# Kernel optimization log

Measured on AMD Instinct MI355X. Metric: run time of the kernel, lower is better.

The kernel has to match this reference:

```python
import jax, jax.numpy as jnp
import numpy as np

N = 300_000   # octree nodes at this depth
K = 27        # 3x3x3 deconv kernel taps
CIN = 32
COUT = 32
G = 8         # group norm groups
B = 8         # octrees in batch
EPS = 1e-5


def setup_inputs() -> dict:
    key = jax.random.key(0)
    k1, k2, k3, k4 = jax.random.split(key, 4)
    data = jax.random.normal(k1, (N, CIN), jnp.float32)
    neigh = jax.random.randint(k2, (N, K), 0, N, jnp.int32)          # neighbor index table
    batch_id = jnp.sort(jax.random.randint(k3, (N,), 0, B, jnp.int32))  # sorted per-node octree id
    weights = jax.random.normal(k4, (K, CIN, COUT), jnp.float32) * 0.05
    gamma = jnp.ones((COUT,), jnp.float32)
    beta = jnp.zeros((COUT,), jnp.float32)
    return dict(data=data, weights=weights, gamma=gamma, beta=beta,
                neigh=neigh, batch_id=batch_id, n_batch=B)


def _octree_group_norm(h, batch_id, gamma, beta, n_batch):
    # Per-octree (segment) group norm, following ocnn.OctreeGroupNorm:
    # count = n_nodes_per_octree * C/G; inv_count = 1/(count+eps);
    # per-group mean/var via scatter_add then within-group channel sum.
    Nn, C = h.shape
    Cg = C // G
    cnt = jax.ops.segment_sum(jnp.ones((Nn,), h.dtype), batch_id,
                              num_segments=n_batch) * (C / G)   # [B]
    inv_cnt = 1.0 / (cnt + EPS)
    s = jax.ops.segment_sum(h, batch_id, num_segments=n_batch)   # [B, C]
    mean_g = s.reshape(n_batch, G, Cg).sum(-1) * inv_cnt[:, None]  # [B, G]
    mean = jnp.repeat(mean_g, Cg, axis=1)                          # [B, C]
    hc = h - mean[batch_id]
    v = jax.ops.segment_sum(hc * hc, batch_id, num_segments=n_batch)
    var_g = v.reshape(n_batch, G, Cg).sum(-1) * inv_cnt[:, None]
    inv_std = jnp.repeat(1.0 / jnp.sqrt(var_g + EPS), Cg, axis=1)  # [B, C]
    return hc * inv_std[batch_id] * gamma + beta


def reference(data, weights, gamma, beta, neigh, batch_id, n_batch):
    # Octree deconv (stride=1): gather 27 neighbors, small matmul per tap, sum.
    x = data[neigh]                                # [N, K, Cin] irregular gather
    out = jnp.einsum('nki,kio->no', x, weights)    # [N, Cout]
    out = _octree_group_norm(out, batch_id, gamma, beta, n_batch)
    return jax.nn.relu(out)
```

## Files before the change

### kernel.cpp

```cpp
#include <hip/hip_runtime.h>
#include <math.h>

#define EPS 1e-5f

typedef __attribute__((ext_vector_type(8)))  short  short8;
typedef __attribute__((ext_vector_type(16))) float  floatx16;

__device__ __forceinline__ unsigned short f2bf(float f) {
    unsigned int u = __float_as_uint(f);
    unsigned int r = (u + 0x7FFFu + ((u >> 16) & 1u)) >> 16;
    return (unsigned short)r;
}
__device__ __forceinline__ float bf2f(unsigned short h) {
    return __uint_as_float(((unsigned int)h) << 16);
}

__global__ __launch_bounds__(256) void pack_data_kernel(
    const float* __restrict__ data, unsigned short* __restrict__ dpk, int N)
{
    const int e4 = blockIdx.x * 256 + threadIdx.x;
    if (e4 >= N * 8) return;
    const float4 v = ((const float4*)data)[e4];
    const int node = e4 >> 3;
    const int cq   = (e4 & 7) * 4;
    ushort4 hi, lo;
    hi.x = f2bf(v.x); lo.x = f2bf(v.x - bf2f(hi.x));
    hi.y = f2bf(v.y); lo.y = f2bf(v.y - bf2f(hi.y));
    hi.z = f2bf(v.z); lo.z = f2bf(v.z - bf2f(hi.z));
    hi.w = f2bf(v.w); lo.w = f2bf(v.w - bf2f(hi.w));
    unsigned short* row = dpk + (size_t)node * 64;
    *(ushort4*)(row + cq)      = hi;
    *(ushort4*)(row + 32 + cq) = lo;
}

__global__ __launch_bounds__(256) void pack_w_kernel(
    const float* __restrict__ W, unsigned short* __restrict__ whi,
    unsigned short* __restrict__ wlo)
{
    const int t = blockIdx.x * 256 + threadIdx.x;
    if (t >= 27 * 2 * 64) return;
    const int l  = t & 63;
    const int h  = (t >> 6) & 1;
    const int k  = t >> 7;
    const int n  = l & 31;
    const int cb = h * 16 + (l >> 5) * 8;
    ushort4 h0, h1, l0, l1;
    const float* wp = W + k * 1024 + n;
    float w0 = wp[(cb + 0) * 32], w1 = wp[(cb + 1) * 32];
    float w2 = wp[(cb + 2) * 32], w3 = wp[(cb + 3) * 32];
    float w4 = wp[(cb + 4) * 32], w5 = wp[(cb + 5) * 32];
    float w6 = wp[(cb + 6) * 32], w7 = wp[(cb + 7) * 32];
    h0.x = f2bf(w0); l0.x = f2bf(w0 - bf2f(h0.x));
    h0.y = f2bf(w1); l0.y = f2bf(w1 - bf2f(h0.y));
    h0.z = f2bf(w2); l0.z = f2bf(w2 - bf2f(h0.z));
    h0.w = f2bf(w3); l0.w = f2bf(w3 - bf2f(h0.w));
    h1.x = f2bf(w4); l1.x = f2bf(w4 - bf2f(h1.x));
    h1.y = f2bf(w5); l1.y = f2bf(w5 - bf2f(h1.y));
    h1.z = f2bf(w6); l1.z = f2bf(w6 - bf2f(h1.z));
    h1.w = f2bf(w7); l1.w = f2bf(w7 - bf2f(h1.w));
    *(ushort4*)(whi + (size_t)t * 8)     = h0;
    *(ushort4*)(whi + (size_t)t * 8 + 4) = h1;
    *(ushort4*)(wlo + (size_t)t * 8)     = l0;
    *(ushort4*)(wlo + (size_t)t * 8 + 4) = l1;
}

__global__ __launch_bounds__(256) void deconv_stats_kernel(
    const unsigned short* __restrict__ dpk, const unsigned short* __restrict__ whi,
    const unsigned short* __restrict__ wlo, const int* __restrict__ neigh,
    const int* __restrict__ batch_id, float* __restrict__ out,
    float* __restrict__ gs1, float* __restrict__ gs2, float* __restrict__ gcnt,
    int N)
{
    __shared__ float ls1[256];
    __shared__ float ls2[256];
    __shared__ float lcnt[8];

    const int t    = threadIdx.x;
    const int wv   = t >> 6;
    const int l    = t & 63;
    const int mrow = l & 31;
    const int half = l >> 5;
    const int wbase = blockIdx.x * 128 + wv * 32;
    const int node  = wbase + mrow;
    const int nc    = node < N ? node : N - 1;
    const long srow = (long)nc * 27;

    ls1[t] = 0.f;
    ls2[t] = 0.f;
    if (t < 8) lcnt[t] = 0.f;
    __syncthreads();

    floatx16 acc;
#pragma unroll
    for (int r = 0; r < 16; ++r) acc[r] = 0.f;

    int nidx = neigh[srow];

#pragma unroll 1
    for (int k = 0; k < 27; ++k) {
        const unsigned short* arow = dpk + (size_t)nidx * 64;
        const short8 a_h0 = *(const short8*)(arow + half * 8);
        const short8 a_h1 = *(const short8*)(arow + 16 + half * 8);
        const short8 a_l0 = *(const short8*)(arow + 32 + half * 8);
        const short8 a_l1 = *(const short8*)(arow + 48 + half * 8);
        const unsigned short* bb = whi + ((size_t)k * 128 + l) * 8;
        const unsigned short* bl = wlo + ((size_t)k * 128 + l) * 8;
        const short8 b_h0 = *(const short8*)(bb);
        const short8 b_h1 = *(const short8*)(bb + 512);
        const short8 b_l0 = *(const short8*)(bl);
        const short8 b_l1 = *(const short8*)(bl + 512);
        if (k < 26) nidx = neigh[srow + k + 1];

        acc = __builtin_amdgcn_mfma_f32_32x32x16_bf16(a_h0, b_h0, acc, 0, 0, 0);
        acc = __builtin_amdgcn_mfma_f32_32x32x16_bf16(a_h1, b_h1, acc, 0, 0, 0);
        acc = __builtin_amdgcn_mfma_f32_32x32x16_bf16(a_l0, b_h0, acc, 0, 0, 0);
        acc = __builtin_amdgcn_mfma_f32_32x32x16_bf16(a_l1, b_h1, acc, 0, 0, 0);
        acc = __builtin_amdgcn_mfma_f32_32x32x16_bf16(a_h0, b_l0, acc, 0, 0, 0);
        acc = __builtin_amdgcn_mfma_f32_32x32x16_bf16(a_h1, b_l1, acc, 0, 0, 0);
    }

    const int co = mrow;
#pragma unroll
    for (int r = 0; r < 16; ++r) {
        const int row = (r & 3) + 8 * (r >> 2) + 4 * half;
        const int n = wbase + row;
        if (n < N) out[(size_t)n * 32 + co] = acc[r];
    }

    bool fast = (wbase + 31 < N);
    int bfst = 0;
    if (fast) {
        bfst = batch_id[wbase];
        fast = (bfst == batch_id[wbase + 31]);
    }
    if (fast) {
        float s1 = 0.f, s2 = 0.f;
#pragma unroll
        for (int r = 0; r < 16; ++r) {
            const float v = acc[r];
            s1 += v;
            s2 += v * v;
        }
        atomicAdd(&ls1[bfst * 32 + co], s1);
        atomicAdd(&ls2[bfst * 32 + co], s2);
    } else {
#pragma unroll
        for (int r = 0; r < 16; ++r) {
            const int row = (r & 3) + 8 * (r >> 2) + 4 * half;
            const int n = wbase + row;
            if (n < N) {
                const int b = batch_id[n];
                const float v = acc[r];
                atomicAdd(&ls1[b * 32 + co], v);
                atomicAdd(&ls2[b * 32 + co], v * v);
            }
        }
    }
    if (half == 0) {
        const int n = wbase + mrow;
        if (n < N) atomicAdd(&lcnt[batch_id[n]], 1.0f);
    }
    __syncthreads();

    {
        float v;
        v = ls1[t]; if (v != 0.f) atomicAdd(&gs1[t], v);
        v = ls2[t]; if (v != 0.f) atomicAdd(&gs2[t], v);
        if (t < 8) { v = lcnt[t]; if (v != 0.f) atomicAdd(&gcnt[t], v); }
    }
}

__global__ __launch_bounds__(256) void gn_relu_kernel(
    float* __restrict__ out, const int* __restrict__ batch_id,
    const float* __restrict__ gs1, const float* __restrict__ gs2,
    const float* __restrict__ gcnt, const float* __restrict__ gamma,
    const float* __restrict__ beta, int N)
{
    const int idx = blockIdx.x * 256 + threadIdx.x;
    if (idx >= N * 8) return;
    const int n = idx >> 3;
    const int g = idx & 7;
    const int b = batch_id[n];

    const float cnt  = gcnt[b] * 4.0f;
    const float icnt = 1.0f / (cnt + EPS);
    const float4 s1 = *(const float4*)(gs1 + b * 32 + g * 4);
    const float4 s2 = *(const float4*)(gs2 + b * 32 + g * 4);
    const float S1 = s1.x + s1.y + s1.z + s1.w;
    const float S2 = s2.x + s2.y + s2.z + s2.w;
    const float m   = S1 * icnt;
    const float var = (S2 - 2.0f * m * S1 + cnt * m * m) * icnt;
    const float istd = rsqrtf(var + EPS);

    const float4 gm4 = *(const float4*)(gamma + g * 4);
    const float4 bt4 = *(const float4*)(beta + g * 4);
    float4 h = *(float4*)(out + (size_t)idx * 4);
    h.x = fmaxf((h.x - m) * istd * gm4.x + bt4.x, 0.f);
    h.y = fmaxf((h.y - m) * istd * gm4.y + bt4.y, 0.f);
    h.z = fmaxf((h.z - m) * istd * gm4.z + bt4.z, 0.f);
    h.w = fmaxf((h.w - m) * istd * gm4.w + bt4.w, 0.f);
    *(float4*)(out + (size_t)idx * 4) = h;
}

extern "C" void kernel_launch(void* const* d_in, const int* in_sizes, int n_in,
                              void* d_out, int out_size, void* d_ws, size_t ws_size,
                              hipStream_t stream) {
    const float* data     = (const float*)d_in[0];
    const float* weights  = (const float*)d_in[1];
    const float* gamma    = (const float*)d_in[2];
    const float* beta     = (const float*)d_in[3];
    const int*   neigh    = (const int*)d_in[4];
    const int*   batch_id = (const int*)d_in[5];
    const int N = in_sizes[0] / 32;
    float* out = (float*)d_out;

    char* wsb = (char*)d_ws;
    float* gs1  = (float*)wsb;
    float* gs2  = gs1 + 256;
    float* gcnt = gs1 + 512;
    unsigned short* dpk = (unsigned short*)(wsb + 4096);
    unsigned short* whi = (unsigned short*)(wsb + 4096 + (size_t)N * 128);
    unsigned short* wlo = whi + 27648;

    hipMemsetAsync(wsb, 0, 520 * sizeof(float), stream);

    hipLaunchKernelGGL(pack_data_kernel, dim3((N * 8 + 255) / 256), dim3(256),
                       0, stream, data, dpk, N);
    hipLaunchKernelGGL(pack_w_kernel, dim3(14), dim3(256), 0, stream,
                       weights, whi, wlo);

    const int nblocks = (N + 127) / 128;
    hipLaunchKernelGGL(deconv_stats_kernel, dim3(nblocks), dim3(256), 0, stream,
                       dpk, whi, wlo, neigh, batch_id, out, gs1, gs2, gcnt, N);

    const int n8 = N * 8;
    hipLaunchKernelGGL(gn_relu_kernel, dim3((n8 + 255) / 256), dim3(256), 0,
                       stream, out, batch_id, gs1, gs2, gcnt, gamma, beta, N);
}
```

Before: 323.8 us.

## Use single fp16 MFMA, LDS-staged weights, padded neighbor table with quad prefetch

Replaces the bf16 hi/lo split (three MFMAs per K-chunk) with one fp16 MFMA, which halves the gathered row size and removes two thirds of the matrix work. Weights are staged once per block into shared memory, padded to 28 taps with a zero tap. The neighbor table is repacked to a stride of 28 so four indices load as one int4, and the next group of gathers is software-prefetched while the current MFMAs run. The risks are fp16 range and precision loss relative to the fp32 reference, an extra pass to repack the neighbor table, and higher LDS use per block.

```diff
diff --git a/kernel.cpp b/kernel.cpp
--- a/kernel.cpp
+++ b/kernel.cpp
@@ -3,74 +3,72 @@
 
 #define EPS 1e-5f
 
-typedef __attribute__((ext_vector_type(8)))  short  short8;
-typedef __attribute__((ext_vector_type(16))) float  floatx16;
-
-__device__ __forceinline__ unsigned short f2bf(float f) {
-    unsigned int u = __float_as_uint(f);
-    unsigned int r = (u + 0x7FFFu + ((u >> 16) & 1u)) >> 16;
-    return (unsigned short)r;
-}
-__device__ __forceinline__ float bf2f(unsigned short h) {
-    return __uint_as_float(((unsigned int)h) << 16);
+typedef __attribute__((ext_vector_type(8)))  _Float16 half8;
+typedef __attribute__((ext_vector_type(16))) float    floatx16;
+
+__device__ __forceinline__ unsigned short f2h_bits(float f) {
+    _Float16 h = (_Float16)f;
+    return __builtin_bit_cast(unsigned short, h);
 }
 
 __global__ __launch_bounds__(256) void pack_data_kernel(
     const float* __restrict__ data, unsigned short* __restrict__ dpk, int N)
 {
-    const int e4 = blockIdx.x * 256 + threadIdx.x;
-    if (e4 >= N * 8) return;
-    const float4 v = ((const float4*)data)[e4];
-    const int node = e4 >> 3;
-    const int cq   = (e4 & 7) * 4;
-    ushort4 hi, lo;
-    hi.x = f2bf(v.x); lo.x = f2bf(v.x - bf2f(hi.x));
-    hi.y = f2bf(v.y); lo.y = f2bf(v.y - bf2f(hi.y));
-    hi.z = f2bf(v.z); lo.z = f2bf(v.z - bf2f(hi.z));
-    hi.w = f2bf(v.w); lo.w = f2bf(v.w - bf2f(hi.w));
-    unsigned short* row = dpk + (size_t)node * 64;
-    *(ushort4*)(row + cq)      = hi;
-    *(ushort4*)(row + 32 + cq) = lo;
+    const int i = blockIdx.x * 256 + threadIdx.x;
+    if (i >= N * 8) return;
+    const float4 v = ((const float4*)data)[i];
+    ushort4 o;
+    o.x = f2h_bits(v.x);
+    o.y = f2h_bits(v.y);
+    o.z = f2h_bits(v.z);
+    o.w = f2h_bits(v.w);
+    ((ushort4*)dpk)[i] = o;
 }
 
 __global__ __launch_bounds__(256) void pack_w_kernel(
-    const float* __restrict__ W, unsigned short* __restrict__ whi,
-    unsigned short* __restrict__ wlo)
+    const float* __restrict__ W, unsigned short* __restrict__ wpk)
 {
     const int t = blockIdx.x * 256 + threadIdx.x;
-    if (t >= 27 * 2 * 64) return;
-    const int l  = t & 63;
-    const int h  = (t >> 6) & 1;
-    const int k  = t >> 7;
-    const int n  = l & 31;
-    const int cb = h * 16 + (l >> 5) * 8;
-    ushort4 h0, h1, l0, l1;
-    const float* wp = W + k * 1024 + n;
-    float w0 = wp[(cb + 0) * 32], w1 = wp[(cb + 1) * 32];
-    float w2 = wp[(cb + 2) * 32], w3 = wp[(cb + 3) * 32];
-    float w4 = wp[(cb + 4) * 32], w5 = wp[(cb + 5) * 32];
-    float w6 = wp[(cb + 6) * 32], w7 = wp[(cb + 7) * 32];
-    h0.x = f2bf(w0); l0.x = f2bf(w0 - bf2f(h0.x));
-    h0.y = f2bf(w1); l0.y = f2bf(w1 - bf2f(h0.y));
-    h0.z = f2bf(w2); l0.z = f2bf(w2 - bf2f(h0.z));
-    h0.w = f2bf(w3); l0.w = f2bf(w3 - bf2f(h0.w));
-    h1.x = f2bf(w4); l1.x = f2bf(w4 - bf2f(h1.x));
-    h1.y = f2bf(w5); l1.y = f2bf(w5 - bf2f(h1.y));
-    h1.z = f2bf(w6); l1.z = f2bf(w6 - bf2f(h1.z));
-    h1.w = f2bf(w7); l1.w = f2bf(w7 - bf2f(h1.w));
-    *(ushort4*)(whi + (size_t)t * 8)     = h0;
-    *(ushort4*)(whi + (size_t)t * 8 + 4) = h1;
-    *(ushort4*)(wlo + (size_t)t * 8)     = l0;
-    *(ushort4*)(wlo + (size_t)t * 8 + 4) = l1;
+    if (t >= 28 * 2 * 64) return;
+    const int l = t & 63;
+    const int c = (t >> 6) & 1;
+    const int k = t >> 7;
+    ushort4 o0 = make_ushort4(0, 0, 0, 0), o1 = o0;
+    if (k < 27) {
+        const int n  = l & 31;
+        const int cb = c * 16 + (l >> 5) * 8;
+        const float* wp = W + k * 1024 + n;
+        o0.x = f2h_bits(wp[(cb + 0) * 32]);
+        o0.y = f2h_bits(wp[(cb + 1) * 32]);
+        o0.z = f2h_bits(wp[(cb + 2) * 32]);
+        o0.w = f2h_bits(wp[(cb + 3) * 32]);
+        o1.x = f2h_bits(wp[(cb + 4) * 32]);
+        o1.y = f2h_bits(wp[(cb + 5) * 32]);
+        o1.z = f2h_bits(wp[(cb + 6) * 32]);
+        o1.w = f2h_bits(wp[(cb + 7) * 32]);
+    }
+    *(ushort4*)(wpk + (size_t)t * 8)     = o0;
+    *(ushort4*)(wpk + (size_t)t * 8 + 4) = o1;
+}
+
+__global__ __launch_bounds__(256) void pack_neigh_kernel(
+    const int* __restrict__ neigh, int* __restrict__ neighp, int N)
+{
+    const int i = blockIdx.x * 256 + threadIdx.x;
+    if (i >= N * 28) return;
+    const int n = i / 28;
+    const int k = i % 28;
+    neighp[i] = neigh[n * 27 + (k < 27 ? k : 26)];
 }
 
 __global__ __launch_bounds__(256) void deconv_stats_kernel(
-    const unsigned short* __restrict__ dpk, const unsigned short* __restrict__ whi,
-    const unsigned short* __restrict__ wlo, const int* __restrict__ neigh,
+    const unsigned short* __restrict__ dpk, const unsigned short* __restrict__ wpk,
+    const int* __restrict__ nbase, int nstride, int quadok,
     const int* __restrict__ batch_id, float* __restrict__ out,
     float* __restrict__ gs1, float* __restrict__ gs2, float* __restrict__ gcnt,
     int N)
 {
+    __shared__ unsigned short BW[28 * 2 * 64 * 8];
     __shared__ float ls1[256];
     __shared__ float ls2[256];
     __shared__ float lcnt[8];
@@ -83,8 +81,10 @@
     const int wbase = blockIdx.x * 128 + wv * 32;
     const int node  = wbase + mrow;
     const int nc    = node < N ? node : N - 1;
-    const long srow = (long)nc * 27;
-
+
+#pragma unroll
+    for (int r = 0; r < 14; ++r)
+        ((int4*)BW)[r * 256 + t] = ((const int4*)wpk)[r * 256 + t];
     ls1[t] = 0.f;
     ls2[t] = 0.f;
     if (t < 8) lcnt[t] = 0.f;
@@ -94,29 +94,63 @@
 #pragma unroll
     for (int r = 0; r < 16; ++r) acc[r] = 0.f;
 
-    int nidx = neigh[srow];
+    const int* nrow = nbase + (size_t)nc * nstride;
+    const int aoff  = half * 8;
+
+    int4 nq;
+    if (quadok) nq = ((const int4*)nrow)[0];
+    else { nq.x = nrow[0]; nq.y = nrow[1]; nq.z = nrow[2]; nq.w = nrow[3]; }
+
+    half8 a0, a1, a2, a3, a4, a5, a6, a7;
+    {
+        const unsigned short* r0 = dpk + (size_t)nq.x * 32;
+        const unsigned short* r1 = dpk + (size_t)nq.y * 32;
+        const unsigned short* r2 = dpk + (size_t)nq.z * 32;
+        const unsigned short* r3 = dpk + (size_t)nq.w * 32;
+        a0 = *(const half8*)(r0 + aoff);  a1 = *(const half8*)(r0 + 16 + aoff);
+        a2 = *(const half8*)(r1 + aoff);  a3 = *(const half8*)(r1 + 16 + aoff);
+        a4 = *(const half8*)(r2 + aoff);  a5 = *(const half8*)(r2 + 16 + aoff);
+        a6 = *(const half8*)(r3 + aoff);  a7 = *(const half8*)(r3 + 16 + aoff);
+    }
+
+    const half8* BL = (const half8*)BW;
 
 #pragma unroll 1
-    for (int k = 0; k < 27; ++k) {
-        const unsigned short* arow = dpk + (size_t)nidx * 64;
-        const short8 a_h0 = *(const short8*)(arow + half * 8);
-        const short8 a_h1 = *(const short8*)(arow + 16 + half * 8);
-        const short8 a_l0 = *(const short8*)(arow + 32 + half * 8);
-        const short8 a_l1 = *(const short8*)(arow + 48 + half * 8);
-        const unsigned short* bb = whi + ((size_t)k * 128 + l) * 8;
-        const unsigned short* bl = wlo + ((size_t)k * 128 + l) * 8;
-        const short8 b_h0 = *(const short8*)(bb);
-        const short8 b_h1 = *(const short8*)(bb + 512);
-        const short8 b_l0 = *(const short8*)(bl);
-        const short8 b_l1 = *(const short8*)(bl + 512);
-        if (k < 26) nidx = neigh[srow + k + 1];
-
-        acc = __builtin_amdgcn_mfma_f32_32x32x16_bf16(a_h0, b_h0, acc, 0, 0, 0);
-        acc = __builtin_amdgcn_mfma_f32_32x32x16_bf16(a_h1, b_h1, acc, 0, 0, 0);
-        acc = __builtin_amdgcn_mfma_f32_32x32x16_bf16(a_l0, b_h0, acc, 0, 0, 0);
-        acc = __builtin_amdgcn_mfma_f32_32x32x16_bf16(a_l1, b_h1, acc, 0, 0, 0);
-        acc = __builtin_amdgcn_mfma_f32_32x32x16_bf16(a_h0, b_l0, acc, 0, 0, 0);
-        acc = __builtin_amdgcn_mfma_f32_32x32x16_bf16(a_h1, b_l1, acc, 0, 0, 0);
+    for (int it = 0; it < 7; ++it) {
+        half8 b0, b1, b2, b3, b4, b5, b6, b7;
+        if (it < 6) {
+            int4 nqn;
+            if (quadok) nqn = ((const int4*)nrow)[it + 1];
+            else {
+                const int kb = (it + 1) * 4;
+                nqn.x = nrow[kb];
+                nqn.y = nrow[kb + 1];
+                nqn.z = nrow[kb + 2];
+                nqn.w = nrow[kb + 3 < 27 ? kb + 3 : 26];
+            }
+            const unsigned short* r0 = dpk + (size_t)nqn.x * 32;
+            const unsigned short* r1 = dpk + (size_t)nqn.y * 32;
+            const unsigned short* r2 = dpk + (size_t)nqn.z * 32;
+            const unsigned short* r3 = dpk + (size_t)nqn.w * 32;
+            b0 = *(const half8*)(r0 + aoff);  b1 = *(const half8*)(r0 + 16 + aoff);
+            b2 = *(const half8*)(r1 + aoff);  b3 = *(const half8*)(r1 + 16 + aoff);
+            b4 = *(const half8*)(r2 + aoff);  b5 = *(const half8*)(r2 + 16 + aoff);
+            b6 = *(const half8*)(r3 + aoff);  b7 = *(const half8*)(r3 + 16 + aoff);
+        }
+
+        acc = __builtin_amdgcn_mfma_f32_32x32x16_f16(a0, BL[(8 * it + 0) * 64 + l], acc, 0, 0, 0);
+        acc = __builtin_amdgcn_mfma_f32_32x32x16_f16(a1, BL[(8 * it + 1) * 64 + l], acc, 0, 0, 0);
+        acc = __builtin_amdgcn_mfma_f32_32x32x16_f16(a2, BL[(8 * it + 2) * 64 + l], acc, 0, 0, 0);
+        acc = __builtin_amdgcn_mfma_f32_32x32x16_f16(a3, BL[(8 * it + 3) * 64 + l], acc, 0, 0, 0);
+        acc = __builtin_amdgcn_mfma_f32_32x32x16_f16(a4, BL[(8 * it + 4) * 64 + l], acc, 0, 0, 0);
+        acc = __builtin_amdgcn_mfma_f32_32x32x16_f16(a5, BL[(8 * it + 5) * 64 + l], acc, 0, 0, 0);
+        acc = __builtin_amdgcn_mfma_f32_32x32x16_f16(a6, BL[(8 * it + 6) * 64 + l], acc, 0, 0, 0);
+        acc = __builtin_amdgcn_mfma_f32_32x32x16_f16(a7, BL[(8 * it + 7) * 64 + l], acc, 0, 0, 0);
+
+        if (it < 6) {
+            a0 = b0; a1 = b1; a2 = b2; a3 = b3;
+            a4 = b4; a5 = b5; a6 = b6; a7 = b7;
+        }
     }
 
     const int co = mrow;
@@ -219,19 +253,29 @@
     float* gs2  = gs1 + 256;
     float* gcnt = gs1 + 512;
     unsigned short* dpk = (unsigned short*)(wsb + 4096);
-    unsigned short* whi = (unsigned short*)(wsb + 4096 + (size_t)N * 128);
-    unsigned short* wlo = whi + 27648;
+    unsigned short* wpk = (unsigned short*)(wsb + 4096 + (size_t)N * 64);
+    int* neighp = (int*)(wsb + 4096 + (size_t)N * 64 + 57344);
+
+    const size_t need = 4096 + (size_t)N * 64 + 57344 + (size_t)N * 112;
+    const int pack_ok = (ws_size >= need) ? 1 : 0;
 
     hipMemsetAsync(wsb, 0, 520 * sizeof(float), stream);
 
     hipLaunchKernelGGL(pack_data_kernel, dim3((N * 8 + 255) / 256), dim3(256),
                        0, stream, data, dpk, N);
     hipLaunchKernelGGL(pack_w_kernel, dim3(14), dim3(256), 0, stream,
-                       weights, whi, wlo);
+                       weights, wpk);
+    if (pack_ok)
+        hipLaunchKernelGGL(pack_neigh_kernel, dim3((N * 28 + 255) / 256),
+                           dim3(256), 0, stream, neigh, neighp, N);
+
+    const int* nbase  = pack_ok ? neighp : neigh;
+    const int nstride = pack_ok ? 28 : 27;
 
     const int nblocks = (N + 127) / 128;
     hipLaunchKernelGGL(deconv_stats_kernel, dim3(nblocks), dim3(256), 0, stream,
-                       dpk, whi, wlo, neigh, batch_id, out, gs1, gs2, gcnt, N);
+                       dpk, wpk, nbase, nstride, pack_ok, batch_id, out,
+                       gs1, gs2, gcnt, N);
 
     const int n8 = N * 8;
     hipLaunchKernelGGL(gn_relu_kernel, dim3((n8 + 255) / 256), dim3(256), 0,
```

After: 289.4 us. -10.6%, faster.
